# Kernel optimization log

Measured on AMD Instinct MI355X. Metric: run time of the kernel, lower is better.

The kernel has to match this reference:

```python
import jax, jax.numpy as jnp
import numpy as np

H, F, E = 256, 512, 8  # hidden_dim, ffn_dim, num_experts


def setup_inputs() -> dict:
    key = jax.random.key(0)
    ks = jax.random.split(key, 7)
    B, S = 8, 4096
    s = lambda fan_in: 1.0 / np.sqrt(fan_in)
    x = jax.random.normal(ks[0], (B, S, H), dtype=jnp.float32)
    Wg = jax.random.uniform(ks[1], (H, E), jnp.float32, -s(H), s(H))
    bg = jnp.zeros((E,), jnp.float32)
    W1 = jax.random.uniform(ks[2], (E, H, F), jnp.float32, -s(H), s(H))
    b1 = jax.random.uniform(ks[3], (E, F), jnp.float32, -s(H), s(H))
    W2 = jax.random.uniform(ks[4], (E, F, H), jnp.float32, -s(F), s(F))
    b2 = jax.random.uniform(ks[5], (E, H), jnp.float32, -s(F), s(F))
    return {"x": x, "Wg": Wg, "bg": bg, "W1": W1, "b1": b1, "W2": W2, "b2": b2}


def reference(x, Wg, bg, W1, b1, W2, b2):
    # gate probabilities over experts: [B,S,E]
    gate_probs = jax.nn.softmax(x @ Wg + bg, axis=-1)
    # all-expert FFN (dense MoE): batched GEMMs over the expert axis
    h = jnp.einsum('bsh,ehf->ebsf', x, W1) + b1[:, None, None, :]   # [E,B,S,F]
    h = jax.nn.gelu(h, approximate=False)                            # torch nn.GELU (erf)
    y = jnp.einsum('ebsf,efh->ebsh', h, W2) + b2[:, None, None, :]  # [E,B,S,H]
    # gate-weighted sum over experts
    mixed = jnp.einsum('ebsh,bse->bsh', y, gate_probs)               # [B,S,H]
    return mixed  # dropout=0.0 / eval mode -> identity
```

## Files before the change

### kernel.cpp

```cpp
#include <hip/hip_runtime.h>
#include <hip/hip_bf16.h>
#include <math.h>

#define H 256
#define F 512
#define E 8
#define T_TOK 32768
#define BM 64
#define FC 64
#define NCH 64

typedef float    f32x4 __attribute__((__ext_vector_type__(4)));
typedef _Float16 f16x8 __attribute__((__ext_vector_type__(8)));
typedef _Float16 f16x4 __attribute__((__ext_vector_type__(4)));

#define BAR_ALL() asm volatile("s_waitcnt vmcnt(0) lgkmcnt(0)\ns_barrier" ::: "memory")

__device__ __forceinline__ void async_copy16(const void* g, void* l) {
    __builtin_amdgcn_global_load_lds((const __attribute__((address_space(1))) void*)g,
                                     (__attribute__((address_space(3))) void*)l, 16, 0, 0);
}

__device__ __forceinline__ float gelu_fast(float v) {
    const float c1 = 2.302117236f;
    const float c2 = 0.102943842f;
    float u2 = v * fmaf(c2, v * v, c1);
    float ex = __builtin_amdgcn_exp2f(u2);
    float r = __builtin_amdgcn_rcpf(ex + 1.0f);
    return v - v * r;
}

__global__ void prep_w1(const float* __restrict__ in, _Float16* __restrict__ out) {
    __shared__ float t[32][33];
    int e = blockIdx.z, f0 = blockIdx.x * 32, h0 = blockIdx.y * 32;
    int tx = threadIdx.x, ty = threadIdx.y;
    const float* ip = in + ((size_t)e * H + h0) * F + f0;
    for (int i = 0; i < 32; i += 8) t[ty + i][tx] = ip[(size_t)(ty + i) * F + tx];
    __syncthreads();
    _Float16* op = out + (size_t)e * F * H;
    for (int i = 0; i < 32; i += 8) {
        int f = f0 + ty + i, h = h0 + tx;
        op[(size_t)f * H + (h ^ ((f & 7) << 3))] = (_Float16)t[tx][ty + i];
    }
}

__global__ void prep_w2p(const float* __restrict__ in, _Float16* __restrict__ out) {
    __shared__ float t[64][65];
    int blk = blockIdx.x;
    int s = blk >> 2, hw = blk & 3;
    int e = s >> 3, c = s & 7;
    int tid = threadIdx.x;
    int fl = tid >> 2, h16 = (tid & 3) * 16;
    const float* ip = in + ((size_t)(e * F + c * 64 + fl)) * H + hw * 64 + h16;
#pragma unroll
    for (int q = 0; q < 4; ++q) {
        float4 v = *(const float4*)(ip + q * 4);
        t[fl][h16 + q * 4 + 0] = v.x;
        t[fl][h16 + q * 4 + 1] = v.y;
        t[fl][h16 + q * 4 + 2] = v.z;
        t[fl][h16 + q * 4 + 3] = v.w;
    }
    __syncthreads();
#pragma unroll
    for (int r = 0; r < 2; ++r) {
        int g = tid * 2 + r;
        int lane = g & 63, iks = g >> 6;
        int fb = (iks & 1) * 32 + (lane >> 4) * 8;
        int hl = (iks >> 1) * 16 + (lane & 15);
        f16x8 v;
#pragma unroll
        for (int d = 0; d < 8; ++d) v[d] = (_Float16)t[fb + d][hl];
        *(f16x8*)(out + (size_t)s * 16384 + ((size_t)hw * 512 + g) * 8) = v;
    }
}

__global__ void gate_kernel(const float* __restrict__ x, const float* __restrict__ Wg,
                            const float* __restrict__ bg, float* __restrict__ probs) {
    int gid = blockIdx.x * blockDim.x + threadIdx.x;
    int t = gid >> 3, e = gid & 7;
    const float* xr = x + (size_t)t * H;
    float acc = 0.f;
    for (int k = 0; k < H; k += 4) {
        float4 xv = *(const float4*)(xr + k);
        acc += xv.x * Wg[(k + 0) * E + e] + xv.y * Wg[(k + 1) * E + e]
             + xv.z * Wg[(k + 2) * E + e] + xv.w * Wg[(k + 3) * E + e];
    }
    acc += bg[e];
    float m = acc;
    for (int s = 1; s < 8; s <<= 1) m = fmaxf(m, __shfl_xor(m, s, 8));
    float p = expf(acc - m);
    float sum = p;
    for (int s = 1; s < 8; s <<= 1) sum += __shfl_xor(sum, s, 8);
    probs[gid] = p / sum;
}

__device__ __forceinline__ void stage_w1(const _Float16* W1t, int s, _Float16* w1d,
                                         int wid, int lane) {
    const char* src = (const char*)W1t + (size_t)s * 32768;
#pragma unroll
    for (int q = 0; q < 4; ++q) {
        int o = (wid * 4 + q) * 1024 + lane * 16;
        async_copy16(src + o, (char*)w1d + o);
    }
}

__global__ __launch_bounds__(512, 4) void moe_main(
    const float* __restrict__ x, const _Float16* __restrict__ W1t,
    const float* __restrict__ b1, const _Float16* __restrict__ W2p,
    const float* __restrict__ b2, const float* __restrict__ probs,
    float* __restrict__ out) {

    __shared__ __align__(16) _Float16 w1s[2][FC * H];
    __shared__ __align__(16) _Float16 hs[2][BM * FC];

    int tid = threadIdx.x;
    int lane = tid & 63, wid = tid >> 6;
    int t0 = blockIdx.x * BM;
    int l15 = lane & 15, l4 = lane >> 4;

    int fw = wid >> 2, tw1 = wid & 3;
    int hw = wid >> 1, tw2 = wid & 1;

    f16x8 xf[8];
    {
        const float* xr = x + (size_t)(t0 + tw1 * 16 + l15) * H + (l4 << 3);
#pragma unroll
        for (int ks = 0; ks < 8; ++ks) {
            float4 v0 = *(const float4*)(xr + ks * 32);
            float4 v1 = *(const float4*)(xr + ks * 32 + 4);
            f16x8 hv;
            hv[0] = (_Float16)v0.x; hv[1] = (_Float16)v0.y; hv[2] = (_Float16)v0.z; hv[3] = (_Float16)v0.w;
            hv[4] = (_Float16)v1.x; hv[5] = (_Float16)v1.y; hv[6] = (_Float16)v1.z; hv[7] = (_Float16)v1.w;
            xf[ks] = hv;
        }
    }
    float pg[8];
    {
        const float* pp = probs + (size_t)(t0 + tw1 * 16 + l15) * E;
        float4 p0 = *(const float4*)pp, p1 = *(const float4*)(pp + 4);
        pg[0] = p0.x; pg[1] = p0.y; pg[2] = p0.z; pg[3] = p0.w;
        pg[4] = p1.x; pg[5] = p1.y; pg[6] = p1.z; pg[7] = p1.w;
    }

    stage_w1(W1t, 0, w1s[0], wid, lane);
    BAR_ALL();

    f32x4 yacc[4][2];
#pragma unroll
    for (int i = 0; i < 4; ++i)
#pragma unroll
        for (int j = 0; j < 2; ++j) yacc[i][j] = (f32x4){0.f, 0.f, 0.f, 0.f};

    for (int s = 0; s < NCH; ++s) {
        int b = s & 1;
        int e = s >> 3, c = s & 7, fbase = c * FC;
        const _Float16* w1p = w1s[b];

        f16x8 av[4][2];
        {
            const _Float16* wb = W2p + (size_t)s * 16384 + ((size_t)(hw * 8) * 64 + lane) * 8;
#pragma unroll
            for (int i = 0; i < 4; ++i) {
                av[i][0] = *(const f16x8*)(wb + (i * 2 + 0) * 512);
                av[i][1] = *(const f16x8*)(wb + (i * 2 + 1) * 512);
            }
        }
        float4 bvq[2];
#pragma unroll
        for (int i = 0; i < 2; ++i)
            bvq[i] = *(const float4*)(b1 + (size_t)e * F + fbase + (fw * 2 + i) * 16 + l4 * 4);

        if (s + 1 < NCH)
            stage_w1(W1t, s + 1, w1s[b ^ 1], wid, lane);

        f32x4 hacc[2];
        hacc[0] = hacc[1] = (f32x4){0.f, 0.f, 0.f, 0.f};
#pragma unroll
        for (int ks = 0; ks < 8; ++ks) {
            int kidx = ks * 32 + (l4 << 3);
            int fr0 = fw * 32 + l15, fr1 = fr0 + 16;
            f16x8 a0 = *(const f16x8*)&w1p[fr0 * H + (kidx ^ ((fr0 & 7) << 3))];
            f16x8 a1 = *(const f16x8*)&w1p[fr1 * H + (kidx ^ ((fr1 & 7) << 3))];
            hacc[0] = __builtin_amdgcn_mfma_f32_16x16x32_f16(a0, xf[ks], hacc[0], 0, 0, 0);
            hacc[1] = __builtin_amdgcn_mfma_f32_16x16x32_f16(a1, xf[ks], hacc[1], 0, 0, 0);
        }

        float p = pg[e];
#pragma unroll
        for (int i = 0; i < 2; ++i) {
            int flocal = (fw * 2 + i) * 16 + l4 * 4;
            float4 bv = bvq[i];
            int tokl = tw1 * 16 + l15;
            f16x4 hp;
            hp[0] = (_Float16)(p * gelu_fast(hacc[i][0] + bv.x));
            hp[1] = (_Float16)(p * gelu_fast(hacc[i][1] + bv.y));
            hp[2] = (_Float16)(p * gelu_fast(hacc[i][2] + bv.z));
            hp[3] = (_Float16)(p * gelu_fast(hacc[i][3] + bv.w));
            int idx = (tokl * FC + flocal) ^ ((tokl & 7) << 3);
            *(f16x4*)&hs[b][idx] = hp;
        }
        BAR_ALL();

#pragma unroll
        for (int ks = 0; ks < FC / 32; ++ks) {
            int kidx = ks * 32 + (l4 << 3);
            f16x8 bv2[2];
#pragma unroll
            for (int j = 0; j < 2; ++j) {
                int tok = tw2 * 32 + j * 16 + l15;
                bv2[j] = *(const f16x8*)&hs[b][(tok * FC + kidx) ^ ((tok & 7) << 3)];
            }
#pragma unroll
            for (int i = 0; i < 4; ++i)
#pragma unroll
                for (int j = 0; j < 2; ++j)
                    yacc[i][j] = __builtin_amdgcn_mfma_f32_16x16x32_f16(av[i][ks], bv2[j], yacc[i][j], 0, 0, 0);
        }
        BAR_ALL();
    }

#pragma unroll
    for (int j = 0; j < 2; ++j) {
        int tok = t0 + tw2 * 32 + j * 16 + l15;
        float pe[8];
#pragma unroll
        for (int e = 0; e < 8; ++e) pe[e] = probs[(size_t)tok * E + e];
#pragma unroll
        for (int i = 0; i < 4; ++i) {
            int h0 = hw * 64 + i * 16 + l4 * 4;
            f32x4 acc = yacc[i][j];
#pragma unroll
            for (int e = 0; e < 8; ++e) {
                float4 b2v = *(const float4*)(b2 + (size_t)e * H + h0);
                acc[0] += pe[e] * b2v.x;
                acc[1] += pe[e] * b2v.y;
                acc[2] += pe[e] * b2v.z;
                acc[3] += pe[e] * b2v.w;
            }
            *(f32x4*)(out + (size_t)tok * H + h0) = acc;
        }
    }
}

extern "C" void kernel_launch(void* const* d_in, const int* in_sizes, int n_in,
                              void* d_out, int out_size, void* d_ws, size_t ws_size,
                              hipStream_t stream) {
    const float* x  = (const float*)d_in[0];
    const float* Wg = (const float*)d_in[1];
    const float* bg = (const float*)d_in[2];
    const float* W1 = (const float*)d_in[3];
    const float* b1 = (const float*)d_in[4];
    const float* W2 = (const float*)d_in[5];
    const float* b2 = (const float*)d_in[6];
    float* out = (float*)d_out;

    _Float16* W1t = (_Float16*)d_ws;
    _Float16* W2p = W1t + (size_t)E * F * H;
    float* probs  = (float*)(W2p + (size_t)64 * 16384);

    dim3 tb(32, 8);
    prep_w1<<<dim3(F / 32, H / 32, E), tb, 0, stream>>>(W1, W1t);
    prep_w2p<<<256, 256, 0, stream>>>(W2, W2p);
    gate_kernel<<<(T_TOK * E) / 256, 256, 0, stream>>>(x, Wg, bg, probs);
    moe_main<<<T_TOK / BM, 512, 0, stream>>>(x, W1t, b1, W2p, b2, probs, out);
}
```

Measured before the change: 262.0 us.

## Double token tile to 128 with 1024 threads and software-pipeline GEMM2 behind GEMM1

Raises the token tile per block from 64 to 128 with 16 waves. Each W1 chunk staged in LDS is now shared across twice as many tokens, and each wave holds a smaller slice of the hidden dimension. The second GEMM for chunk s-1 is moved ahead of the first GEMM for chunk s, with one tail iteration after the loop. This removes one barrier per iteration and overlaps the two GEMMs. The W2 pre-pack layout is reordered to match the new per-wave fragment indexing. The cost is larger blocks with higher register pressure under launch_bounds(1024,4), which could reduce occupancy or cause spills.

```diff
diff --git a/kernel.cpp b/kernel.cpp
--- a/kernel.cpp
+++ b/kernel.cpp
@@ -6,7 +6,7 @@
 #define F 512
 #define E 8
 #define T_TOK 32768
-#define BM 64
+#define BM 128
 #define FC 64
 #define NCH 64
 
@@ -47,30 +47,33 @@
 __global__ void prep_w2p(const float* __restrict__ in, _Float16* __restrict__ out) {
     __shared__ float t[64][65];
     int blk = blockIdx.x;
-    int s = blk >> 2, hw = blk & 3;
+    int s = blk >> 2, q = blk & 3;
     int e = s >> 3, c = s & 7;
     int tid = threadIdx.x;
     int fl = tid >> 2, h16 = (tid & 3) * 16;
-    const float* ip = in + ((size_t)(e * F + c * 64 + fl)) * H + hw * 64 + h16;
-#pragma unroll
-    for (int q = 0; q < 4; ++q) {
-        float4 v = *(const float4*)(ip + q * 4);
-        t[fl][h16 + q * 4 + 0] = v.x;
-        t[fl][h16 + q * 4 + 1] = v.y;
-        t[fl][h16 + q * 4 + 2] = v.z;
-        t[fl][h16 + q * 4 + 3] = v.w;
+    const float* ip = in + ((size_t)(e * F + c * 64 + fl)) * H + q * 64 + h16;
+#pragma unroll
+    for (int w = 0; w < 4; ++w) {
+        float4 v = *(const float4*)(ip + w * 4);
+        t[fl][h16 + w * 4 + 0] = v.x;
+        t[fl][h16 + w * 4 + 1] = v.y;
+        t[fl][h16 + w * 4 + 2] = v.z;
+        t[fl][h16 + w * 4 + 3] = v.w;
     }
     __syncthreads();
 #pragma unroll
     for (int r = 0; r < 2; ++r) {
-        int g = tid * 2 + r;
-        int lane = g & 63, iks = g >> 6;
-        int fb = (iks & 1) * 32 + (lane >> 4) * 8;
-        int hl = (iks >> 1) * 16 + (lane & 15);
+        int g2 = tid * 2 + r;
+        int htl = g2 >> 7;
+        int rem = g2 & 127;
+        int ks = rem >> 6, lane = rem & 63;
+        int fb = ks * 32 + (lane >> 4) * 8;
+        int hl = htl * 16 + (lane & 15);
         f16x8 v;
 #pragma unroll
         for (int d = 0; d < 8; ++d) v[d] = (_Float16)t[fb + d][hl];
-        *(f16x8*)(out + (size_t)s * 16384 + ((size_t)hw * 512 + g) * 8) = v;
+        int G = ((q * 4 + htl) * 2 + ks) * 64 + lane;
+        *(f16x8*)(out + (size_t)s * 16384 + (size_t)G * 8) = v;
     }
 }
 
@@ -98,13 +101,13 @@
                                          int wid, int lane) {
     const char* src = (const char*)W1t + (size_t)s * 32768;
 #pragma unroll
-    for (int q = 0; q < 4; ++q) {
-        int o = (wid * 4 + q) * 1024 + lane * 16;
+    for (int q = 0; q < 2; ++q) {
+        int o = (wid * 2 + q) * 1024 + lane * 16;
         async_copy16(src + o, (char*)w1d + o);
     }
 }
 
-__global__ __launch_bounds__(512, 4) void moe_main(
+__global__ __launch_bounds__(1024, 4) void moe_main(
     const float* __restrict__ x, const _Float16* __restrict__ W1t,
     const float* __restrict__ b1, const _Float16* __restrict__ W2p,
     const float* __restrict__ b2, const float* __restrict__ probs,
@@ -118,7 +121,7 @@
     int t0 = blockIdx.x * BM;
     int l15 = lane & 15, l4 = lane >> 4;
 
-    int fw = wid >> 2, tw1 = wid & 3;
+    int fw = wid >> 3, tw1 = wid & 7;
     int hw = wid >> 1, tw2 = wid & 1;
 
     f16x8 xf[8];
@@ -145,33 +148,52 @@
     stage_w1(W1t, 0, w1s[0], wid, lane);
     BAR_ALL();
 
-    f32x4 yacc[4][2];
-#pragma unroll
-    for (int i = 0; i < 4; ++i)
-#pragma unroll
-        for (int j = 0; j < 2; ++j) yacc[i][j] = (f32x4){0.f, 0.f, 0.f, 0.f};
+    f32x4 yacc[2][4];
+#pragma unroll
+    for (int i = 0; i < 2; ++i)
+#pragma unroll
+        for (int j = 0; j < 4; ++j) yacc[i][j] = (f32x4){0.f, 0.f, 0.f, 0.f};
+
+    f16x8 av[2][2];
 
     for (int s = 0; s < NCH; ++s) {
         int b = s & 1;
         int e = s >> 3, c = s & 7, fbase = c * FC;
         const _Float16* w1p = w1s[b];
 
-        f16x8 av[4][2];
+        if (s + 1 < NCH)
+            stage_w1(W1t, s + 1, w1s[b ^ 1], wid, lane);
+
+        if (s > 0) {
+#pragma unroll
+            for (int ks = 0; ks < 2; ++ks) {
+                int kidx = ks * 32 + (l4 << 3);
+                f16x8 bv2[4];
+#pragma unroll
+                for (int j = 0; j < 4; ++j) {
+                    int tok = tw2 * 64 + j * 16 + l15;
+                    bv2[j] = *(const f16x8*)&hs[b ^ 1][(tok * FC + kidx) ^ ((tok & 7) << 3)];
+                }
+#pragma unroll
+                for (int i = 0; i < 2; ++i)
+#pragma unroll
+                    for (int j = 0; j < 4; ++j)
+                        yacc[i][j] = __builtin_amdgcn_mfma_f32_16x16x32_f16(av[i][ks], bv2[j], yacc[i][j], 0, 0, 0);
+            }
+        }
+
         {
-            const _Float16* wb = W2p + (size_t)s * 16384 + ((size_t)(hw * 8) * 64 + lane) * 8;
-#pragma unroll
-            for (int i = 0; i < 4; ++i) {
-                av[i][0] = *(const f16x8*)(wb + (i * 2 + 0) * 512);
-                av[i][1] = *(const f16x8*)(wb + (i * 2 + 1) * 512);
-            }
+            const _Float16* wb = W2p + (size_t)s * 16384 + (size_t)lane * 8;
+#pragma unroll
+            for (int i = 0; i < 2; ++i)
+#pragma unroll
+                for (int ks = 0; ks < 2; ++ks)
+                    av[i][ks] = *(const f16x8*)(wb + (((hw * 2 + i) * 2 + ks) * 64) * 8);
         }
         float4 bvq[2];
 #pragma unroll
         for (int i = 0; i < 2; ++i)
             bvq[i] = *(const float4*)(b1 + (size_t)e * F + fbase + (fw * 2 + i) * 16 + l4 * 4);
-
-        if (s + 1 < NCH)
-            stage_w1(W1t, s + 1, w1s[b ^ 1], wid, lane);
 
         f32x4 hacc[2];
         hacc[0] = hacc[1] = (f32x4){0.f, 0.f, 0.f, 0.f};
@@ -199,35 +221,38 @@
             int idx = (tokl * FC + flocal) ^ ((tokl & 7) << 3);
             *(f16x4*)&hs[b][idx] = hp;
         }
+
         BAR_ALL();
-
-#pragma unroll
-        for (int ks = 0; ks < FC / 32; ++ks) {
+    }
+
+    {
+        int b = (NCH - 1) & 1;
+#pragma unroll
+        for (int ks = 0; ks < 2; ++ks) {
             int kidx = ks * 32 + (l4 << 3);
-            f16x8 bv2[2];
-#pragma unroll
-            for (int j = 0; j < 2; ++j) {
-                int tok = tw2 * 32 + j * 16 + l15;
+            f16x8 bv2[4];
+#pragma unroll
+            for (int j = 0; j < 4; ++j) {
+                int tok = tw2 * 64 + j * 16 + l15;
                 bv2[j] = *(const f16x8*)&hs[b][(tok * FC + kidx) ^ ((tok & 7) << 3)];
             }
 #pragma unroll
-            for (int i = 0; i < 4; ++i)
-#pragma unroll
-                for (int j = 0; j < 2; ++j)
+            for (int i = 0; i < 2; ++i)
+#pragma unroll
+                for (int j = 0; j < 4; ++j)
                     yacc[i][j] = __builtin_amdgcn_mfma_f32_16x16x32_f16(av[i][ks], bv2[j], yacc[i][j], 0, 0, 0);
         }
-        BAR_ALL();
-    }
-
-#pragma unroll
-    for (int j = 0; j < 2; ++j) {
-        int tok = t0 + tw2 * 32 + j * 16 + l15;
+    }
+
+#pragma unroll
+    for (int j = 0; j < 4; ++j) {
+        int tok = t0 + tw2 * 64 + j * 16 + l15;
         float pe[8];
 #pragma unroll
         for (int e = 0; e < 8; ++e) pe[e] = probs[(size_t)tok * E + e];
 #pragma unroll
-        for (int i = 0; i < 4; ++i) {
-            int h0 = hw * 64 + i * 16 + l4 * 4;
+        for (int i = 0; i < 2; ++i) {
+            int h0 = hw * 32 + i * 16 + l4 * 4;
             f32x4 acc = yacc[i][j];
 #pragma unroll
             for (int e = 0; e < 8; ++e) {
@@ -262,5 +287,5 @@
     prep_w1<<<dim3(F / 32, H / 32, E), tb, 0, stream>>>(W1, W1t);
     prep_w2p<<<256, 256, 0, stream>>>(W2, W2p);
     gate_kernel<<<(T_TOK * E) / 256, 256, 0, stream>>>(x, Wg, bg, probs);
-    moe_main<<<T_TOK / BM, 512, 0, stream>>>(x, W1t, b1, W2p, b2, probs, out);
-}
+    moe_main<<<T_TOK / BM, 1024, 0, stream>>>(x, W1t, b1, W2p, b2, probs, out);
+}
```

Measured after the change: 243.1 us. -7.2%, faster.

## Double token tile and load W1 fragments directly from global in MFMA layout

Applied to the files above, without the earlier changes.

The token tile per block grows from 64 to 128, so each weight fragment feeds twice as many MFMAs. W1 is prepacked into a per-lane MFMA fragment layout and loaded straight from global/L2 into registers, which removes the LDS staging buffer and its async copies. The second barrier per chunk is dropped, relying on the double-buffered hs array, and the barrier now waits only on LDS. Register pressure rises (launch bounds drop to 2 blocks per SIMD) and the grid halves to 256 blocks, which lowers occupancy and may leave the CUs underfilled.

```diff
diff --git a/kernel.cpp b/kernel.cpp
--- a/kernel.cpp
+++ b/kernel.cpp
@@ -6,7 +6,7 @@
 #define F 512
 #define E 8
 #define T_TOK 32768
-#define BM 64
+#define BM 128
 #define FC 64
 #define NCH 64
 
@@ -14,12 +14,7 @@
 typedef _Float16 f16x8 __attribute__((__ext_vector_type__(8)));
 typedef _Float16 f16x4 __attribute__((__ext_vector_type__(4)));
 
-#define BAR_ALL() asm volatile("s_waitcnt vmcnt(0) lgkmcnt(0)\ns_barrier" ::: "memory")
-
-__device__ __forceinline__ void async_copy16(const void* g, void* l) {
-    __builtin_amdgcn_global_load_lds((const __attribute__((address_space(1))) void*)g,
-                                     (__attribute__((address_space(3))) void*)l, 16, 0, 0);
-}
+#define BAR_LG() asm volatile("s_waitcnt lgkmcnt(0)\ns_barrier" ::: "memory")
 
 __device__ __forceinline__ float gelu_fast(float v) {
     const float c1 = 2.302117236f;
@@ -30,17 +25,33 @@
     return v - v * r;
 }
 
-__global__ void prep_w1(const float* __restrict__ in, _Float16* __restrict__ out) {
-    __shared__ float t[32][33];
-    int e = blockIdx.z, f0 = blockIdx.x * 32, h0 = blockIdx.y * 32;
-    int tx = threadIdx.x, ty = threadIdx.y;
-    const float* ip = in + ((size_t)e * H + h0) * F + f0;
-    for (int i = 0; i < 32; i += 8) t[ty + i][tx] = ip[(size_t)(ty + i) * F + tx];
+__global__ void prep_w1p(const float* __restrict__ in, _Float16* __restrict__ out) {
+    __shared__ float t[256][33];
+    int blk = blockIdx.x;
+    int s = blk >> 1, fw = blk & 1;
+    int e = s >> 3, c = s & 7;
+    int f0 = c * 64 + fw * 32;
+    int tid = threadIdx.x;
+    int hr = tid >> 3, q = tid & 7;
+#pragma unroll
+    for (int pp = 0; pp < 8; ++pp) {
+        int h = pp * 32 + hr;
+        float4 v = *(const float4*)(in + ((size_t)e * H + h) * F + f0 + q * 4);
+        t[h][q * 4 + 0] = v.x;
+        t[h][q * 4 + 1] = v.y;
+        t[h][q * 4 + 2] = v.z;
+        t[h][q * 4 + 3] = v.w;
+    }
     __syncthreads();
-    _Float16* op = out + (size_t)e * F * H;
-    for (int i = 0; i < 32; i += 8) {
-        int f = f0 + ty + i, h = h0 + tx;
-        op[(size_t)f * H + (h ^ ((f & 7) << 3))] = (_Float16)t[tx][ty + i];
+#pragma unroll
+    for (int r = 0; r < 4; ++r) {
+        int g = r * 256 + tid;
+        int ks = g >> 7, pair = (g >> 6) & 1, ln = g & 63;
+        int l4v = ln >> 4, l15v = ln & 15;
+        f16x8 v;
+#pragma unroll
+        for (int d = 0; d < 8; ++d) v[d] = (_Float16)t[ks * 32 + l4v * 8 + d][pair * 16 + l15v];
+        *(f16x8*)(out + ((size_t)blk * 1024 + g) * 8) = v;
     }
 }
 
@@ -94,23 +105,12 @@
     probs[gid] = p / sum;
 }
 
-__device__ __forceinline__ void stage_w1(const _Float16* W1t, int s, _Float16* w1d,
-                                         int wid, int lane) {
-    const char* src = (const char*)W1t + (size_t)s * 32768;
-#pragma unroll
-    for (int q = 0; q < 4; ++q) {
-        int o = (wid * 4 + q) * 1024 + lane * 16;
-        async_copy16(src + o, (char*)w1d + o);
-    }
-}
-
-__global__ __launch_bounds__(512, 4) void moe_main(
-    const float* __restrict__ x, const _Float16* __restrict__ W1t,
+__global__ __launch_bounds__(512, 2) void moe_main(
+    const float* __restrict__ x, const _Float16* __restrict__ W1p,
     const float* __restrict__ b1, const _Float16* __restrict__ W2p,
     const float* __restrict__ b2, const float* __restrict__ probs,
     float* __restrict__ out) {
 
-    __shared__ __align__(16) _Float16 w1s[2][FC * H];
     __shared__ __align__(16) _Float16 hs[2][BM * FC];
 
     int tid = threadIdx.x;
@@ -121,9 +121,10 @@
     int fw = wid >> 2, tw1 = wid & 3;
     int hw = wid >> 1, tw2 = wid & 1;
 
-    f16x8 xf[8];
-    {
-        const float* xr = x + (size_t)(t0 + tw1 * 16 + l15) * H + (l4 << 3);
+    f16x8 xf[8][2];
+#pragma unroll
+    for (int j = 0; j < 2; ++j) {
+        const float* xr = x + (size_t)(t0 + tw1 * 32 + j * 16 + l15) * H + (l4 << 3);
 #pragma unroll
         for (int ks = 0; ks < 8; ++ks) {
             float4 v0 = *(const float4*)(xr + ks * 32);
@@ -131,31 +132,35 @@
             f16x8 hv;
             hv[0] = (_Float16)v0.x; hv[1] = (_Float16)v0.y; hv[2] = (_Float16)v0.z; hv[3] = (_Float16)v0.w;
             hv[4] = (_Float16)v1.x; hv[5] = (_Float16)v1.y; hv[6] = (_Float16)v1.z; hv[7] = (_Float16)v1.w;
-            xf[ks] = hv;
-        }
-    }
-    float pg[8];
-    {
-        const float* pp = probs + (size_t)(t0 + tw1 * 16 + l15) * E;
-        float4 p0 = *(const float4*)pp, p1 = *(const float4*)(pp + 4);
-        pg[0] = p0.x; pg[1] = p0.y; pg[2] = p0.z; pg[3] = p0.w;
-        pg[4] = p1.x; pg[5] = p1.y; pg[6] = p1.z; pg[7] = p1.w;
-    }
-
-    stage_w1(W1t, 0, w1s[0], wid, lane);
-    BAR_ALL();
-
-    f32x4 yacc[4][2];
+            xf[ks][j] = hv;
+        }
+    }
+
+    f32x4 yacc[4][4];
 #pragma unroll
     for (int i = 0; i < 4; ++i)
 #pragma unroll
-        for (int j = 0; j < 2; ++j) yacc[i][j] = (f32x4){0.f, 0.f, 0.f, 0.f};
+        for (int j = 0; j < 4; ++j) yacc[i][j] = (f32x4){0.f, 0.f, 0.f, 0.f};
+
+    float p0g = 0.f, p1g = 0.f;
 
     for (int s = 0; s < NCH; ++s) {
         int b = s & 1;
         int e = s >> 3, c = s & 7, fbase = c * FC;
-        const _Float16* w1p = w1s[b];
-
+
+        if ((s & 7) == 0) {
+            p0g = probs[(size_t)(t0 + tw1 * 32 + l15) * E + e];
+            p1g = probs[(size_t)(t0 + tw1 * 32 + 16 + l15) * E + e];
+        }
+
+        const _Float16* w1b = W1p + ((size_t)(s * 2 + fw) * 1024 + lane) * 8;
+
+        f16x8 w1a[4][2];
+#pragma unroll
+        for (int ks = 0; ks < 4; ++ks) {
+            w1a[ks][0] = *(const f16x8*)(w1b + (ks * 2 + 0) * 512);
+            w1a[ks][1] = *(const f16x8*)(w1b + (ks * 2 + 1) * 512);
+        }
         f16x8 av[4][2];
         {
             const _Float16* wb = W2p + (size_t)s * 16384 + ((size_t)(hw * 8) * 64 + lane) * 8;
@@ -170,58 +175,69 @@
         for (int i = 0; i < 2; ++i)
             bvq[i] = *(const float4*)(b1 + (size_t)e * F + fbase + (fw * 2 + i) * 16 + l4 * 4);
 
-        if (s + 1 < NCH)
-            stage_w1(W1t, s + 1, w1s[b ^ 1], wid, lane);
-
-        f32x4 hacc[2];
-        hacc[0] = hacc[1] = (f32x4){0.f, 0.f, 0.f, 0.f};
-#pragma unroll
-        for (int ks = 0; ks < 8; ++ks) {
-            int kidx = ks * 32 + (l4 << 3);
-            int fr0 = fw * 32 + l15, fr1 = fr0 + 16;
-            f16x8 a0 = *(const f16x8*)&w1p[fr0 * H + (kidx ^ ((fr0 & 7) << 3))];
-            f16x8 a1 = *(const f16x8*)&w1p[fr1 * H + (kidx ^ ((fr1 & 7) << 3))];
-            hacc[0] = __builtin_amdgcn_mfma_f32_16x16x32_f16(a0, xf[ks], hacc[0], 0, 0, 0);
-            hacc[1] = __builtin_amdgcn_mfma_f32_16x16x32_f16(a1, xf[ks], hacc[1], 0, 0, 0);
-        }
-
-        float p = pg[e];
+        f32x4 hacc[2][2];
+        hacc[0][0] = hacc[0][1] = hacc[1][0] = hacc[1][1] = (f32x4){0.f, 0.f, 0.f, 0.f};
+#pragma unroll
+        for (int ks = 0; ks < 4; ++ks) {
+            hacc[0][0] = __builtin_amdgcn_mfma_f32_16x16x32_f16(w1a[ks][0], xf[ks][0], hacc[0][0], 0, 0, 0);
+            hacc[0][1] = __builtin_amdgcn_mfma_f32_16x16x32_f16(w1a[ks][0], xf[ks][1], hacc[0][1], 0, 0, 0);
+            hacc[1][0] = __builtin_amdgcn_mfma_f32_16x16x32_f16(w1a[ks][1], xf[ks][0], hacc[1][0], 0, 0, 0);
+            hacc[1][1] = __builtin_amdgcn_mfma_f32_16x16x32_f16(w1a[ks][1], xf[ks][1], hacc[1][1], 0, 0, 0);
+        }
+#pragma unroll
+        for (int ks = 0; ks < 4; ++ks) {
+            w1a[ks][0] = *(const f16x8*)(w1b + ((ks + 4) * 2 + 0) * 512);
+            w1a[ks][1] = *(const f16x8*)(w1b + ((ks + 4) * 2 + 1) * 512);
+        }
+#pragma unroll
+        for (int ks = 0; ks < 4; ++ks) {
+            hacc[0][0] = __builtin_amdgcn_mfma_f32_16x16x32_f16(w1a[ks][0], xf[ks + 4][0], hacc[0][0], 0, 0, 0);
+            hacc[0][1] = __builtin_amdgcn_mfma_f32_16x16x32_f16(w1a[ks][0], xf[ks + 4][1], hacc[0][1], 0, 0, 0);
+            hacc[1][0] = __builtin_amdgcn_mfma_f32_16x16x32_f16(w1a[ks][1], xf[ks + 4][0], hacc[1][0], 0, 0, 0);
+            hacc[1][1] = __builtin_amdgcn_mfma_f32_16x16x32_f16(w1a[ks][1], xf[ks + 4][1], hacc[1][1], 0, 0, 0);
+        }
+
 #pragma unroll
         for (int i = 0; i < 2; ++i) {
             int flocal = (fw * 2 + i) * 16 + l4 * 4;
             float4 bv = bvq[i];
-            int tokl = tw1 * 16 + l15;
-            f16x4 hp;
-            hp[0] = (_Float16)(p * gelu_fast(hacc[i][0] + bv.x));
-            hp[1] = (_Float16)(p * gelu_fast(hacc[i][1] + bv.y));
-            hp[2] = (_Float16)(p * gelu_fast(hacc[i][2] + bv.z));
-            hp[3] = (_Float16)(p * gelu_fast(hacc[i][3] + bv.w));
-            int idx = (tokl * FC + flocal) ^ ((tokl & 7) << 3);
-            *(f16x4*)&hs[b][idx] = hp;
-        }
-        BAR_ALL();
+#pragma unroll
+            for (int j = 0; j < 2; ++j) {
+                int tokl = tw1 * 32 + j * 16 + l15;
+                float p = j ? p1g : p0g;
+                f32x4 hv = hacc[i][j];
+                f16x4 hp;
+                hp[0] = (_Float16)(p * gelu_fast(hv[0] + bv.x));
+                hp[1] = (_Float16)(p * gelu_fast(hv[1] + bv.y));
+                hp[2] = (_Float16)(p * gelu_fast(hv[2] + bv.z));
+                hp[3] = (_Float16)(p * gelu_fast(hv[3] + bv.w));
+                int idx = (tokl * FC + flocal) ^ ((tokl & 7) << 3);
+                *(f16x4*)&hs[b][idx] = hp;
+            }
+        }
+
+        BAR_LG();
 
 #pragma unroll
         for (int ks = 0; ks < FC / 32; ++ks) {
             int kidx = ks * 32 + (l4 << 3);
-            f16x8 bv2[2];
-#pragma unroll
-            for (int j = 0; j < 2; ++j) {
-                int tok = tw2 * 32 + j * 16 + l15;
+            f16x8 bv2[4];
+#pragma unroll
+            for (int j = 0; j < 4; ++j) {
+                int tok = tw2 * 64 + j * 16 + l15;
                 bv2[j] = *(const f16x8*)&hs[b][(tok * FC + kidx) ^ ((tok & 7) << 3)];
             }
 #pragma unroll
             for (int i = 0; i < 4; ++i)
 #pragma unroll
-                for (int j = 0; j < 2; ++j)
+                for (int j = 0; j < 4; ++j)
                     yacc[i][j] = __builtin_amdgcn_mfma_f32_16x16x32_f16(av[i][ks], bv2[j], yacc[i][j], 0, 0, 0);
         }
-        BAR_ALL();
-    }
-
-#pragma unroll
-    for (int j = 0; j < 2; ++j) {
-        int tok = t0 + tw2 * 32 + j * 16 + l15;
+    }
+
+#pragma unroll
+    for (int j = 0; j < 4; ++j) {
+        int tok = t0 + tw2 * 64 + j * 16 + l15;
         float pe[8];
 #pragma unroll
         for (int e = 0; e < 8; ++e) pe[e] = probs[(size_t)tok * E + e];
@@ -254,13 +270,12 @@
     const float* b2 = (const float*)d_in[6];
     float* out = (float*)d_out;
 
-    _Float16* W1t = (_Float16*)d_ws;
-    _Float16* W2p = W1t + (size_t)E * F * H;
+    _Float16* W1p = (_Float16*)d_ws;
+    _Float16* W2p = W1p + (size_t)E * F * H;
     float* probs  = (float*)(W2p + (size_t)64 * 16384);
 
-    dim3 tb(32, 8);
-    prep_w1<<<dim3(F / 32, H / 32, E), tb, 0, stream>>>(W1, W1t);
+    prep_w1p<<<128, 256, 0, stream>>>(W1, W1p);
     prep_w2p<<<256, 256, 0, stream>>>(W2, W2p);
     gate_kernel<<<(T_TOK * E) / 256, 256, 0, stream>>>(x, Wg, bg, probs);
-    moe_main<<<T_TOK / BM, 512, 0, stream>>>(x, W1t, b1, W2p, b2, probs, out);
-}
+    moe_main<<<T_TOK / BM, 512, 0, stream>>>(x, W1p, b1, W2p, b2, probs, out);
+}
```

Result: faster. 217.6 us, median of 2 (-17.0%).
